# Performance work log

Measured on AMD Instinct MI355X. Metric: run time of the kernel, lower is better.

The kernel has to match this reference:

```python
import jax, jax.numpy as jnp
import numpy as np

USER_SIZE = 100000
EMBED_DIM = 512
BATCH, SEQ = 16, 2048
N_NODES = BATCH * SEQ          # 32768, adj is [N_NODES, N_NODES]
NNZ = N_NODES * 32             # avg degree 32
LN_EPS = 1e-5


def setup_inputs() -> dict:
    key = jax.random.key(0)
    ks = jax.random.split(key, 6)
    user_ids = jax.random.randint(ks[0], (BATCH, SEQ), 0, USER_SIZE, dtype=jnp.int32)
    adj_row = jax.random.randint(ks[1], (NNZ,), 0, N_NODES, dtype=jnp.int32)
    adj_col = jax.random.randint(ks[2], (NNZ,), 0, N_NODES, dtype=jnp.int32)
    # normalized-adjacency-like positive values, scaled ~1/degree to keep outputs stable
    adj_vals = jax.random.uniform(ks[3], (NNZ,), dtype=jnp.float32) / 32.0
    embedding = jax.random.normal(ks[4], (USER_SIZE, EMBED_DIM), dtype=jnp.float32) * 0.02
    W = jax.random.normal(ks[5], (EMBED_DIM, EMBED_DIM), dtype=jnp.float32) * 0.05
    bias = jnp.zeros((EMBED_DIM,), dtype=jnp.float32)
    ln_gamma = jnp.ones((EMBED_DIM,), dtype=jnp.float32)
    ln_beta = jnp.zeros((EMBED_DIM,), dtype=jnp.float32)
    return {"user_ids": user_ids, "adj_row": adj_row, "adj_col": adj_col,
            "adj_vals": adj_vals, "embedding": embedding, "W": W, "bias": bias,
            "ln_gamma": ln_gamma, "ln_beta": ln_beta}


def reference(user_ids, adj_row, adj_col, adj_vals, embedding, W, bias, ln_gamma, ln_beta):
    # Embedding lookup: [B, S, D]
    x = embedding[user_ids]
    # GCN on flattened nodes: support = X @ W, then sparse adj @ support + bias
    flat = x.reshape(N_NODES, EMBED_DIM)
    support = flat @ W                                  # [N, D]
    msgs = adj_vals[:, None] * support[adj_col]          # [nnz, D]
    agg = jax.ops.segment_sum(msgs, adj_row, num_segments=N_NODES)  # sparse.mm
    out = (agg + bias).reshape(BATCH, SEQ, EMBED_DIM)
    # LayerNorm over last dim
    mu = jnp.mean(out, axis=-1, keepdims=True)
    var = jnp.var(out, axis=-1, keepdims=True)
    out = (out - mu) * jax.lax.rsqrt(var + LN_EPS) * ln_gamma + ln_beta
    # Dropout is identity in eval mode
    return out
```

## Files before the change

kernel.cpp:

```cpp
#include <hip/hip_runtime.h>

#define N_NODES 32768
#define EMBED   512
#define NNZ_TOT 1048576
#define LN_EPS  1e-5f

typedef __attribute__((ext_vector_type(8))) short bf16x8;
typedef __attribute__((ext_vector_type(4))) float f32x4;
typedef __attribute__((ext_vector_type(4))) unsigned int u32x4;

__device__ __forceinline__ unsigned short f2bf(float x) {
    unsigned int u = __float_as_uint(x);
    unsigned int r = u + 0x7fffu + ((u >> 16) & 1u);
    return (unsigned short)(r >> 16);
}
__device__ __forceinline__ unsigned int pk2(float a, float b) {
    return (unsigned int)f2bf(a) | ((unsigned int)f2bf(b) << 16);
}

__global__ void zero_ints(int* __restrict__ p, int n) {
    int i = blockIdx.x * blockDim.x + threadIdx.x;
    if (i < n) p[i] = 0;
}

__global__ __launch_bounds__(256) void wt_kernel(
    const float* __restrict__ W, unsigned short* __restrict__ Wt)
{
    __shared__ float tile[32][33];
    const int tx = threadIdx.x & 31, ty = threadIdx.x >> 5;
    const int kb = blockIdx.y * 32, nb = blockIdx.x * 32;
#pragma unroll
    for (int i = 0; i < 32; i += 8)
        tile[ty + i][tx] = W[(long)(kb + ty + i) * EMBED + nb + tx];
    __syncthreads();
#pragma unroll
    for (int i = 0; i < 32; i += 8)
        Wt[(long)(nb + ty + i) * EMBED + kb + tx] = f2bf(tile[tx][ty + i]);
}

__global__ __launch_bounds__(256) void gemm_mfma(
    const int* __restrict__ uids, const float* __restrict__ emb,
    const unsigned short* __restrict__ Wt, unsigned short* __restrict__ support)
{
    __shared__ unsigned short As[128][40];
    __shared__ unsigned short Bs[128][40];

    const int t  = threadIdx.x;
    const int m0 = blockIdx.y * 128;
    const int n0 = blockIdx.x * 128;

    const int wave = t >> 6;
    const int lane = t & 63;
    const int wm   = (wave & 1) * 64;
    const int wn   = (wave >> 1) * 64;
    const int l16  = lane & 15;
    const int quad = lane >> 4;

    const int srow  = t >> 1;
    const int shalf = (t & 1) * 16;
    const int uid   = uids[m0 + srow];
    const float* arow = emb + (long)uid * EMBED + shalf;
    const unsigned short* brow = Wt + (long)(n0 + srow) * EMBED + shalf;

    f32x4 acc[4][4] = {};

    for (int k0 = 0; k0 < EMBED; k0 += 32) {
        const float4* ap = (const float4*)(arow + k0);
        float4 v0 = ap[0], v1 = ap[1], v2 = ap[2], v3 = ap[3];
        u32x4 lo, hi;
        lo.x = pk2(v0.x, v0.y); lo.y = pk2(v0.z, v0.w);
        lo.z = pk2(v1.x, v1.y); lo.w = pk2(v1.z, v1.w);
        hi.x = pk2(v2.x, v2.y); hi.y = pk2(v2.z, v2.w);
        hi.z = pk2(v3.x, v3.y); hi.w = pk2(v3.z, v3.w);
        *(u32x4*)&As[srow][shalf]     = lo;
        *(u32x4*)&As[srow][shalf + 8] = hi;
        const u32x4* bp = (const u32x4*)(brow + k0);
        *(u32x4*)&Bs[srow][shalf]     = bp[0];
        *(u32x4*)&Bs[srow][shalf + 8] = bp[1];
        __syncthreads();

        bf16x8 af[4], bfr[4];
#pragma unroll
        for (int i = 0; i < 4; ++i)
            af[i] = *(const bf16x8*)&As[wm + i * 16 + l16][quad * 8];
#pragma unroll
        for (int j = 0; j < 4; ++j)
            bfr[j] = *(const bf16x8*)&Bs[wn + j * 16 + l16][quad * 8];
#pragma unroll
        for (int i = 0; i < 4; ++i)
#pragma unroll
            for (int j = 0; j < 4; ++j)
                acc[i][j] = __builtin_amdgcn_mfma_f32_16x16x32_bf16(af[i], bfr[j], acc[i][j], 0, 0, 0);
        __syncthreads();
    }

#pragma unroll
    for (int i = 0; i < 4; ++i) {
#pragma unroll
        for (int j = 0; j < 4; ++j) {
            const int col = n0 + wn + j * 16 + l16;
#pragma unroll
            for (int r = 0; r < 4; ++r) {
                const int row = m0 + wm + i * 16 + quad * 4 + r;
                support[(long)row * EMBED + col] = f2bf(acc[i][j][r]);
            }
        }
    }
}

__global__ void hist_kernel(const int* __restrict__ adj_row, int* __restrict__ counts) {
    int i = blockIdx.x * blockDim.x + threadIdx.x;
    if (i < NNZ_TOT) atomicAdd(&counts[adj_row[i]], 1);
}

__global__ __launch_bounds__(1024) void scan_kernel(
    const int* __restrict__ counts, int* __restrict__ row_start)
{
    __shared__ int ssum[1024];
    const int t = threadIdx.x;
    const int base = t * 32;
    int loc[32];
    int run = 0;
#pragma unroll
    for (int i = 0; i < 32; ++i) {
        int c = counts[base + i];
        loc[i] = run;
        run += c;
    }
    ssum[t] = run;
    __syncthreads();
    for (int off = 1; off < 1024; off <<= 1) {
        int v = (t >= off) ? ssum[t - off] : 0;
        __syncthreads();
        ssum[t] += v;
        __syncthreads();
    }
    int prefix = (t > 0) ? ssum[t - 1] : 0;
#pragma unroll
    for (int i = 0; i < 32; ++i) row_start[base + i] = prefix + loc[i];
    if (t == 1023) row_start[N_NODES] = ssum[1023];
}

__global__ void scatter_kernel(
    const int* __restrict__ adj_row, const int* __restrict__ adj_col,
    const float* __restrict__ adj_vals, const int* __restrict__ row_start,
    int* __restrict__ cursor, int2* __restrict__ sc)
{
    int i = blockIdx.x * blockDim.x + threadIdx.x;
    if (i < NNZ_TOT) {
        int r = adj_row[i];
        int pos = atomicAdd(&cursor[r], 1);
        sc[row_start[r] + pos] = make_int2(adj_col[i], __float_as_int(adj_vals[i]));
    }
}

__global__ __launch_bounds__(256) void agg_ln_v2(
    const int* __restrict__ row_start, const int2* __restrict__ sc,
    const unsigned short* __restrict__ support,
    const float* __restrict__ bias, const float* __restrict__ gamma,
    const float* __restrict__ beta, float* __restrict__ out)
{
    const int n = blockIdx.x;
    const int t = threadIdx.x;
    const int w = t >> 6;
    const int l = t & 63;
    const int s = row_start[n];
    const int e = row_start[n + 1];

    const unsigned short* supp_l = support + l * 8;

    float acc[8] = {};
    int i = s + w;
    for (; i + 4 < e; i += 8) {
        int2 p0 = sc[i];
        int2 p1 = sc[i + 4];
        u32x4 u0 = *(const u32x4*)(supp_l + p0.x * EMBED);
        u32x4 u1 = *(const u32x4*)(supp_l + p1.x * EMBED);
        float v0 = __int_as_float(p0.y);
        float v1 = __int_as_float(p1.y);
#pragma unroll
        for (int j = 0; j < 4; ++j) {
            unsigned int a = u0[j];
            acc[2 * j]     = fmaf(v0, __uint_as_float(a << 16), acc[2 * j]);
            acc[2 * j + 1] = fmaf(v0, __uint_as_float(a & 0xffff0000u), acc[2 * j + 1]);
        }
#pragma unroll
        for (int j = 0; j < 4; ++j) {
            unsigned int a = u1[j];
            acc[2 * j]     = fmaf(v1, __uint_as_float(a << 16), acc[2 * j]);
            acc[2 * j + 1] = fmaf(v1, __uint_as_float(a & 0xffff0000u), acc[2 * j + 1]);
        }
    }
    if (i < e) {
        int2 p0 = sc[i];
        u32x4 u0 = *(const u32x4*)(supp_l + p0.x * EMBED);
        float v0 = __int_as_float(p0.y);
#pragma unroll
        for (int j = 0; j < 4; ++j) {
            unsigned int a = u0[j];
            acc[2 * j]     = fmaf(v0, __uint_as_float(a << 16), acc[2 * j]);
            acc[2 * j + 1] = fmaf(v0, __uint_as_float(a & 0xffff0000u), acc[2 * j + 1]);
        }
    }

    __shared__ float part[4][EMBED];
    *(f32x4*)&part[w][l * 8]     = *(f32x4*)&acc[0];
    *(f32x4*)&part[w][l * 8 + 4] = *(f32x4*)&acc[4];
    __syncthreads();

    const int d = t * 2;
    float x0 = part[0][d] + part[1][d] + part[2][d] + part[3][d] + bias[d];
    float x1 = part[0][d + 1] + part[1][d + 1] + part[2][d + 1] + part[3][d + 1] + bias[d + 1];

    float s1 = x0 + x1;
    float s2 = x0 * x0 + x1 * x1;
#pragma unroll
    for (int off = 32; off > 0; off >>= 1) {
        s1 += __shfl_down(s1, off, 64);
        s2 += __shfl_down(s2, off, 64);
    }
    __shared__ float ws1[4], ws2[4];
    const int wid = t >> 6, lane = t & 63;
    if (lane == 0) { ws1[wid] = s1; ws2[wid] = s2; }
    __syncthreads();
    if (t == 0) {
        ws1[0] = ws1[0] + ws1[1] + ws1[2] + ws1[3];
        ws2[0] = ws2[0] + ws2[1] + ws2[2] + ws2[3];
    }
    __syncthreads();
    const float mean = ws1[0] * (1.f / 512.f);
    const float var  = ws2[0] * (1.f / 512.f) - mean * mean;
    const float rstd = rsqrtf(var + LN_EPS);

    float2 o;
    o.x = (x0 - mean) * rstd * gamma[d] + beta[d];
    o.y = (x1 - mean) * rstd * gamma[d + 1] + beta[d + 1];
    *(float2*)&out[(long)n * EMBED + d] = o;
}

extern "C" void kernel_launch(void* const* d_in, const int* in_sizes, int n_in,
                              void* d_out, int out_size, void* d_ws, size_t ws_size,
                              hipStream_t stream)
{
    const int*   user_ids = (const int*)  d_in[0];
    const int*   adj_row  = (const int*)  d_in[1];
    const int*   adj_col  = (const int*)  d_in[2];
    const float* adj_vals = (const float*)d_in[3];
    const float* emb      = (const float*)d_in[4];
    const float* W        = (const float*)d_in[5];
    const float* bias     = (const float*)d_in[6];
    const float* gamma    = (const float*)d_in[7];
    const float* beta     = (const float*)d_in[8];
    float* out = (float*)d_out;

    char* ws = (char*)d_ws;
    size_t off = 0;
    unsigned short* support = (unsigned short*)(ws + off); off += (size_t)N_NODES * EMBED * 2;
    unsigned short* Wt      = (unsigned short*)(ws + off); off += (size_t)EMBED * EMBED * 2;
    int2*  sc        = (int2*) (ws + off); off += (size_t)NNZ_TOT * 8;
    int*   row_start = (int*)  (ws + off); off += (size_t)(N_NODES + 4) * 4;
    int*   counts    = (int*)  (ws + off); off += (size_t)N_NODES * 4;
    int*   cursor    = (int*)  (ws + off); off += (size_t)N_NODES * 4;
    (void)off; (void)ws_size; (void)in_sizes; (void)n_in; (void)out_size;

    zero_ints<<<(2 * N_NODES + 255) / 256, 256, 0, stream>>>(counts, 2 * N_NODES);

    wt_kernel<<<dim3(16, 16), 256, 0, stream>>>(W, Wt);

    gemm_mfma<<<dim3(EMBED / 128, N_NODES / 128), 256, 0, stream>>>(user_ids, emb, Wt, support);

    hist_kernel<<<NNZ_TOT / 256, 256, 0, stream>>>(adj_row, counts);
    scan_kernel<<<1, 1024, 0, stream>>>(counts, row_start);
    scatter_kernel<<<NNZ_TOT / 256, 256, 0, stream>>>(adj_row, adj_col, adj_vals,
                                                      row_start, cursor, sc);

    agg_ln_v2<<<N_NODES, 256, 0, stream>>>(row_start, sc, support,
                                           bias, gamma, beta, out);
}
```

Before: 553.9 us.

## Double-buffer GEMM LDS tiles and vectorize histogram, scan, and scatter kernels

The GEMM now double-buffers its shared-memory A/B tiles. Loads for the next K slice are issued before the MFMAs on the current slice, which removes one barrier per iteration. The histogram, scan and scatter kernels now read adj_row, adj_col, adj_vals and counts as 4-wide vectors, with each thread handling four edges, so fewer threads are launched. These changes raise register and LDS use in the GEMM, and the vectorized kernels rely on NNZ being divisible by 4 with aligned buffers.

```diff
diff --git a/kernel.cpp b/kernel.cpp
--- a/kernel.cpp
+++ b/kernel.cpp
@@ -42,8 +42,8 @@
     const int* __restrict__ uids, const float* __restrict__ emb,
     const unsigned short* __restrict__ Wt, unsigned short* __restrict__ support)
 {
-    __shared__ unsigned short As[128][40];
-    __shared__ unsigned short Bs[128][40];
+    __shared__ unsigned short As[2][128][40];
+    __shared__ unsigned short Bs[2][128][40];
 
     const int t  = threadIdx.x;
     const int m0 = blockIdx.y * 128;
@@ -64,34 +64,61 @@
 
     f32x4 acc[4][4] = {};
 
-    for (int k0 = 0; k0 < EMBED; k0 += 32) {
-        const float4* ap = (const float4*)(arow + k0);
+    {
+        const float4* ap = (const float4*)arow;
         float4 v0 = ap[0], v1 = ap[1], v2 = ap[2], v3 = ap[3];
+        const u32x4* bp = (const u32x4*)brow;
+        u32x4 b0 = bp[0], b1 = bp[1];
         u32x4 lo, hi;
         lo.x = pk2(v0.x, v0.y); lo.y = pk2(v0.z, v0.w);
         lo.z = pk2(v1.x, v1.y); lo.w = pk2(v1.z, v1.w);
         hi.x = pk2(v2.x, v2.y); hi.y = pk2(v2.z, v2.w);
         hi.z = pk2(v3.x, v3.y); hi.w = pk2(v3.z, v3.w);
-        *(u32x4*)&As[srow][shalf]     = lo;
-        *(u32x4*)&As[srow][shalf + 8] = hi;
-        const u32x4* bp = (const u32x4*)(brow + k0);
-        *(u32x4*)&Bs[srow][shalf]     = bp[0];
-        *(u32x4*)&Bs[srow][shalf + 8] = bp[1];
-        __syncthreads();
+        *(u32x4*)&As[0][srow][shalf]     = lo;
+        *(u32x4*)&As[0][srow][shalf + 8] = hi;
+        *(u32x4*)&Bs[0][srow][shalf]     = b0;
+        *(u32x4*)&Bs[0][srow][shalf + 8] = b1;
+    }
+    __syncthreads();
+
+    for (int k = 0; k < 16; ++k) {
+        const int cur = k & 1;
+
+        float4 nv0, nv1, nv2, nv3;
+        u32x4 nb0, nb1;
+        if (k < 15) {
+            const float4* ap = (const float4*)(arow + (k + 1) * 32);
+            nv0 = ap[0]; nv1 = ap[1]; nv2 = ap[2]; nv3 = ap[3];
+            const u32x4* bp = (const u32x4*)(brow + (k + 1) * 32);
+            nb0 = bp[0]; nb1 = bp[1];
+        }
 
         bf16x8 af[4], bfr[4];
 #pragma unroll
         for (int i = 0; i < 4; ++i)
-            af[i] = *(const bf16x8*)&As[wm + i * 16 + l16][quad * 8];
+            af[i] = *(const bf16x8*)&As[cur][wm + i * 16 + l16][quad * 8];
 #pragma unroll
         for (int j = 0; j < 4; ++j)
-            bfr[j] = *(const bf16x8*)&Bs[wn + j * 16 + l16][quad * 8];
+            bfr[j] = *(const bf16x8*)&Bs[cur][wn + j * 16 + l16][quad * 8];
 #pragma unroll
         for (int i = 0; i < 4; ++i)
 #pragma unroll
             for (int j = 0; j < 4; ++j)
                 acc[i][j] = __builtin_amdgcn_mfma_f32_16x16x32_bf16(af[i], bfr[j], acc[i][j], 0, 0, 0);
-        __syncthreads();
+
+        if (k < 15) {
+            u32x4 lo, hi;
+            lo.x = pk2(nv0.x, nv0.y); lo.y = pk2(nv0.z, nv0.w);
+            lo.z = pk2(nv1.x, nv1.y); lo.w = pk2(nv1.z, nv1.w);
+            hi.x = pk2(nv2.x, nv2.y); hi.y = pk2(nv2.z, nv2.w);
+            hi.z = pk2(nv3.x, nv3.y); hi.w = pk2(nv3.z, nv3.w);
+            const int nxt = cur ^ 1;
+            *(u32x4*)&As[nxt][srow][shalf]     = lo;
+            *(u32x4*)&As[nxt][srow][shalf + 8] = hi;
+            *(u32x4*)&Bs[nxt][srow][shalf]     = nb0;
+            *(u32x4*)&Bs[nxt][srow][shalf + 8] = nb1;
+            __syncthreads();
+        }
     }
 
 #pragma unroll
@@ -108,9 +135,13 @@
     }
 }
 
-__global__ void hist_kernel(const int* __restrict__ adj_row, int* __restrict__ counts) {
+__global__ void hist_kernel(const int4* __restrict__ adj_row4, int* __restrict__ counts) {
     int i = blockIdx.x * blockDim.x + threadIdx.x;
-    if (i < NNZ_TOT) atomicAdd(&counts[adj_row[i]], 1);
+    int4 r = adj_row4[i];
+    atomicAdd(&counts[r.x], 1);
+    atomicAdd(&counts[r.y], 1);
+    atomicAdd(&counts[r.z], 1);
+    atomicAdd(&counts[r.w], 1);
 }
 
 __global__ __launch_bounds__(1024) void scan_kernel(
@@ -121,11 +152,14 @@
     const int base = t * 32;
     int loc[32];
     int run = 0;
-#pragma unroll
-    for (int i = 0; i < 32; ++i) {
-        int c = counts[base + i];
-        loc[i] = run;
-        run += c;
+    const int4* c4 = (const int4*)(counts + base);
+#pragma unroll
+    for (int i = 0; i < 8; ++i) {
+        int4 c = c4[i];
+        loc[4 * i]     = run; run += c.x;
+        loc[4 * i + 1] = run; run += c.y;
+        loc[4 * i + 2] = run; run += c.z;
+        loc[4 * i + 3] = run; run += c.w;
     }
     ssum[t] = run;
     __syncthreads();
@@ -142,16 +176,19 @@
 }
 
 __global__ void scatter_kernel(
-    const int* __restrict__ adj_row, const int* __restrict__ adj_col,
-    const float* __restrict__ adj_vals, const int* __restrict__ row_start,
+    const int4* __restrict__ adj_row4, const int4* __restrict__ adj_col4,
+    const float4* __restrict__ adj_vals4, const int* __restrict__ row_start,
     int* __restrict__ cursor, int2* __restrict__ sc)
 {
     int i = blockIdx.x * blockDim.x + threadIdx.x;
-    if (i < NNZ_TOT) {
-        int r = adj_row[i];
-        int pos = atomicAdd(&cursor[r], 1);
-        sc[row_start[r] + pos] = make_int2(adj_col[i], __float_as_int(adj_vals[i]));
-    }
+    int4  r = adj_row4[i];
+    int4  c = adj_col4[i];
+    float4 v = adj_vals4[i];
+    int p;
+    p = atomicAdd(&cursor[r.x], 1); sc[row_start[r.x] + p] = make_int2(c.x, __float_as_int(v.x));
+    p = atomicAdd(&cursor[r.y], 1); sc[row_start[r.y] + p] = make_int2(c.y, __float_as_int(v.y));
+    p = atomicAdd(&cursor[r.z], 1); sc[row_start[r.z] + p] = make_int2(c.z, __float_as_int(v.z));
+    p = atomicAdd(&cursor[r.w], 1); sc[row_start[r.w] + p] = make_int2(c.w, __float_as_int(v.w));
 }
 
 __global__ __launch_bounds__(256) void agg_ln_v2(
@@ -269,10 +306,11 @@
 
     gemm_mfma<<<dim3(EMBED / 128, N_NODES / 128), 256, 0, stream>>>(user_ids, emb, Wt, support);
 
-    hist_kernel<<<NNZ_TOT / 256, 256, 0, stream>>>(adj_row, counts);
+    hist_kernel<<<NNZ_TOT / 4 / 256, 256, 0, stream>>>((const int4*)adj_row, counts);
     scan_kernel<<<1, 1024, 0, stream>>>(counts, row_start);
-    scatter_kernel<<<NNZ_TOT / 256, 256, 0, stream>>>(adj_row, adj_col, adj_vals,
-                                                      row_start, cursor, sc);
+    scatter_kernel<<<NNZ_TOT / 4 / 256, 256, 0, stream>>>((const int4*)adj_row, (const int4*)adj_col,
+                                                          (const float4*)adj_vals,
+                                                          row_start, cursor, sc);
 
     agg_ln_v2<<<N_NODES, 256, 0, stream>>>(row_start, sc, support,
                                            bias, gamma, beta, out);
```

After: 558.0 us. No clear change (+0.8%).
